# Optimization experiments

Measured on AMD Instinct MI355X. Metric: run time of the kernel, lower is better.

## Reference

```python
import jax, jax.numpy as jnp
import numpy as np

N_NODES = 50000
N_EDGES = 1600000
IN_CH = 128
OUT_CH = 32
HEADS = 4
NEG_SLOPE = 0.2

def setup_inputs() -> dict:
    key = jax.random.key(0)
    ks = jax.random.split(key, 6)
    x = jax.random.normal(ks[0], (N_NODES, IN_CH), dtype=jnp.float32)
    edge_index = jax.random.randint(ks[1], (2, N_EDGES), 0, N_NODES, dtype=jnp.int64)
    # GATConv parameters (glorot-ish scale)
    W = jax.random.normal(ks[2], (IN_CH, HEADS * OUT_CH), dtype=jnp.float32) * (1.0 / np.sqrt(IN_CH))
    att_src = jax.random.normal(ks[3], (HEADS, OUT_CH), dtype=jnp.float32) * (1.0 / np.sqrt(OUT_CH))
    att_dst = jax.random.normal(ks[4], (HEADS, OUT_CH), dtype=jnp.float32) * (1.0 / np.sqrt(OUT_CH))
    bias = jnp.zeros((HEADS * OUT_CH,), dtype=jnp.float32)
    return {"x": x, "edge_index": edge_index, "W": W, "att_src": att_src, "att_dst": att_dst, "bias": bias}

def reference(x, edge_index, W, att_src, att_dst, bias):
    N = x.shape[0]
    H, C = att_src.shape
    # PyG default: add self loops
    loop = jnp.arange(N, dtype=edge_index.dtype)
    src = jnp.concatenate([edge_index[0], loop])  # [E+N]
    dst = jnp.concatenate([edge_index[1], loop])  # [E+N]
    # linear projection -> [N, H, C]
    h = (x @ W).reshape(N, H, C)
    # per-node attention contributions [N, H]
    a_src = jnp.einsum('nhc,hc->nh', h, att_src)
    a_dst = jnp.einsum('nhc,hc->nh', h, att_dst)
    # edge-wise logits with LeakyReLU [E', H]
    alpha = jax.nn.leaky_relu(a_src[src] + a_dst[dst], negative_slope=NEG_SLOPE)
    # segment softmax over incoming edges of each dst node
    amax = jax.ops.segment_max(alpha, dst, num_segments=N)
    alpha = jnp.exp(alpha - amax[dst])
    denom = jax.ops.segment_sum(alpha, dst, num_segments=N)
    alpha = alpha / (denom[dst] + 1e-16)
    # weighted scatter-aggregate of source features [N, H, C]
    msg = h[src] * alpha[..., None]
    out = jax.ops.segment_sum(msg, dst, num_segments=N)
    out = out.reshape(N, H * C) + bias  # concat heads + bias
    return out, alpha
```

## Files before the change

### kernel.cpp

```cpp
#include <hip/hip_runtime.h>
#include <math.h>

#define N_NODES 50000
#define N_EDGES 1600000
#define E_TOT   1650000
#define GROWS   32
#define GEMM_BLOCKS ((N_NODES + GROWS - 1) / GROWS)
#define STRIDE  72
#define NBKT    391
#define PPART   450
#define EPB     3556
#define CAP     32
#define NALPHA  ((E_TOT + 255) / 256)

__device__ __forceinline__ unsigned short f2bf(float f) {
    unsigned int b = __float_as_uint(f);
    return (unsigned short)((b + 0x7FFFu + ((b >> 16) & 1u)) >> 16);
}
__device__ __forceinline__ float bf_lo(unsigned int u) {
    return __uint_as_float(u << 16);
}
__device__ __forceinline__ float bf_hi(unsigned int u) {
    return __uint_as_float(u & 0xFFFF0000u);
}

__global__ __launch_bounds__(256) void k_gemm_part(
    const float* __restrict__ x, const float* __restrict__ W,
    const float* __restrict__ att_src, const float* __restrict__ att_dst,
    unsigned short* __restrict__ hbuf16, float* __restrict__ asrc,
    float* __restrict__ adst,
    const int* __restrict__ esrc, const int* __restrict__ edst,
    unsigned int* __restrict__ cells, int* __restrict__ cellCnt)
{
    __shared__ float  xs[GROWS * 128];
    __shared__ float4 Wl[64 * 32];
    __shared__ int    cur[NBKT];
    const int tid = threadIdx.x;

    if (blockIdx.x >= PPART) {
        const int n0 = (blockIdx.x - PPART) * GROWS;

        {
            const float4* xg = (const float4*)x;
            float4* xs4 = (float4*)xs;
            #pragma unroll
            for (int i = 0; i < 4; i++) {
                int idx = tid + 256 * i;
                int row = n0 + (idx >> 5);
                int col = idx & 31;
                row = min(row, N_NODES - 1);
                xs4[idx] = xg[(size_t)row * 32 + col];
            }
        }

        const int ct = tid & 31;
        const int rt = tid >> 5;
        const int rb = rt * 4;

        float acc[4][4];
        #pragma unroll
        for (int r = 0; r < 4; r++)
            #pragma unroll
            for (int q = 0; q < 4; q++) acc[r][q] = 0.f;

        const float4* W4  = (const float4*)W;
        const float4* xs4 = (const float4*)xs;
        #pragma unroll
        for (int kc = 0; kc < 2; kc++) {
            const float4* Wg = W4 + kc * 2048;
            __syncthreads();
            #pragma unroll
            for (int i = 0; i < 8; i++)
                Wl[tid + 256 * i] = Wg[tid + 256 * i];
            __syncthreads();

            const int kq = kc * 16;
            #pragma unroll 2
            for (int k4 = 0; k4 < 16; k4++) {
                float4 w0 = Wl[(k4 * 4 + 0) * 32 + ct];
                float4 w1 = Wl[(k4 * 4 + 1) * 32 + ct];
                float4 w2 = Wl[(k4 * 4 + 2) * 32 + ct];
                float4 w3 = Wl[(k4 * 4 + 3) * 32 + ct];
                #pragma unroll
                for (int r = 0; r < 4; r++) {
                    float4 xv = xs4[(rb + r) * 32 + kq + k4];
                    acc[r][0] = fmaf(xv.x, w0.x, acc[r][0]);
                    acc[r][1] = fmaf(xv.x, w0.y, acc[r][1]);
                    acc[r][2] = fmaf(xv.x, w0.z, acc[r][2]);
                    acc[r][3] = fmaf(xv.x, w0.w, acc[r][3]);
                    acc[r][0] = fmaf(xv.y, w1.x, acc[r][0]);
                    acc[r][1] = fmaf(xv.y, w1.y, acc[r][1]);
                    acc[r][2] = fmaf(xv.y, w1.z, acc[r][2]);
                    acc[r][3] = fmaf(xv.y, w1.w, acc[r][3]);
                    acc[r][0] = fmaf(xv.z, w2.x, acc[r][0]);
                    acc[r][1] = fmaf(xv.z, w2.y, acc[r][1]);
                    acc[r][2] = fmaf(xv.z, w2.z, acc[r][2]);
                    acc[r][3] = fmaf(xv.z, w2.w, acc[r][3]);
                    acc[r][0] = fmaf(xv.w, w3.x, acc[r][0]);
                    acc[r][1] = fmaf(xv.w, w3.y, acc[r][1]);
                    acc[r][2] = fmaf(xv.w, w3.z, acc[r][2]);
                    acc[r][3] = fmaf(xv.w, w3.w, acc[r][3]);
                }
            }
        }

        ushort4* h4 = (ushort4*)hbuf16;
        #pragma unroll
        for (int r = 0; r < 4; r++) {
            int row = n0 + rb + r;
            if (row < N_NODES) {
                ushort4 p;
                p.x = f2bf(acc[r][0]); p.y = f2bf(acc[r][1]);
                p.z = f2bf(acc[r][2]); p.w = f2bf(acc[r][3]);
                h4[(size_t)row * 32 + ct] = p;
            }
        }

        const int head = ct >> 3;
        const int c0   = (ct & 7) * 4;
        const float* As = att_src + head * 32 + c0;
        const float* Ad = att_dst + head * 32 + c0;
        float sv[4], dv[4];
        #pragma unroll
        for (int r = 0; r < 4; r++) {
            sv[r] = acc[r][0]*As[0] + acc[r][1]*As[1] + acc[r][2]*As[2] + acc[r][3]*As[3];
            dv[r] = acc[r][0]*Ad[0] + acc[r][1]*Ad[1] + acc[r][2]*Ad[2] + acc[r][3]*Ad[3];
        }
        #pragma unroll
        for (int off = 4; off >= 1; off >>= 1) {
            #pragma unroll
            for (int r = 0; r < 4; r++) {
                sv[r] += __shfl_down(sv[r], off, 8);
                dv[r] += __shfl_down(dv[r], off, 8);
            }
        }
        if ((ct & 7) == 0) {
            #pragma unroll
            for (int r = 0; r < 4; r++) {
                int row = n0 + rb + r;
                if (row < N_NODES) {
                    asrc[row * 4 + head] = sv[r];
                    adst[row * 4 + head] = dv[r];
                }
            }
        }
    } else {
        const int p = blockIdx.x;
        for (int i = tid; i < NBKT; i += 256) cur[i] = 0;
        __syncthreads();

        const int base = p * EPB;
        const int end  = min(base + EPB, N_EDGES);
        unsigned int* myCells = cells + (size_t)p * NBKT * CAP;
        for (int e = base + tid; e < end; e += 256) {
            int d = edst[e];
            int s = esrc[e];
            int bkt = d >> 7;
            int pos = atomicAdd(&cur[bkt], 1);
            if (pos < CAP)
                myCells[bkt * CAP + pos] = ((unsigned int)(d & 127) << 16) | (unsigned int)s;
        }
        __syncthreads();
        for (int i = tid; i < NBKT; i += 256)
            cellCnt[p * NBKT + i] = min(cur[i], CAP);
    }
}

__global__ __launch_bounds__(512) void k_build(
    const unsigned int* __restrict__ cells, const int* __restrict__ cellCnt,
    const float4* __restrict__ asrc, const float4* __restrict__ adst,
    int* __restrict__ csr, int* __restrict__ cnt, float4* __restrict__ rden)
{
    __shared__ int cur[128];
    __shared__ int scnt[PPART];
    __shared__ __align__(16) int rows[128 * STRIDE];

    const int tid = threadIdx.x;
    const int b   = blockIdx.x;
    const int d0  = b * 128;
    const int ndst = min(128, N_NODES - d0);
    for (int i = tid; i < 128; i += 512) cur[i] = 0;
    for (int i = tid; i < PPART; i += 512) scnt[i] = cellCnt[i * NBKT + b];
    __syncthreads();

    for (int slot = tid; slot < PPART * CAP; slot += 512) {
        int p = slot >> 5;
        int j = slot & 31;
        if (j < scnt[p]) {
            unsigned int v = cells[((size_t)p * NBKT + b) * CAP + j];
            int dlo = (int)(v >> 16);
            int s   = (int)(v & 0xFFFFu);
            int r = atomicAdd(&cur[dlo], 1);
            if (r < STRIDE) rows[dlo * STRIDE + r] = s;
        }
    }
    __syncthreads();

    int4* dst4 = (int4*)(csr + (size_t)d0 * STRIDE);
    const int4* src4 = (const int4*)rows;
    const int n4 = ndst * (STRIDE / 4);
    for (int k = tid; k < n4; k += 512) dst4[k] = src4[k];
    for (int t = tid; t < ndst; t += 512) cnt[d0 + t] = min(cur[t], STRIDE);

    const int g = tid >> 5, l = tid & 31;
    for (int dd = g; dd < ndst; dd += 16) {
        const int dn = d0 + dd;
        const float4 b4 = adst[dn];
        const int c = min(cur[dd], STRIDE);
        float4 dp = make_float4(0.f, 0.f, 0.f, 0.f);
        for (int i = l; i <= c; i += 32) {
            int s = (i < c) ? rows[dd * STRIDE + i] : dn;
            float4 a4 = asrc[s];
            float l0=a4.x+b4.x, l1=a4.y+b4.y, l2=a4.z+b4.z, l3=a4.w+b4.w;
            l0=fmaxf(l0,0.2f*l0); l1=fmaxf(l1,0.2f*l1);
            l2=fmaxf(l2,0.2f*l2); l3=fmaxf(l3,0.2f*l3);
            dp.x += __expf(l0); dp.y += __expf(l1);
            dp.z += __expf(l2); dp.w += __expf(l3);
        }
        #pragma unroll
        for (int o = 16; o >= 1; o >>= 1) {
            dp.x += __shfl_down(dp.x, o, 32);
            dp.y += __shfl_down(dp.y, o, 32);
            dp.z += __shfl_down(dp.z, o, 32);
            dp.w += __shfl_down(dp.w, o, 32);
        }
        if (l == 0) {
            float4 r;
            r.x = 1.0f / (dp.x + 1e-16f);
            r.y = 1.0f / (dp.y + 1e-16f);
            r.z = 1.0f / (dp.z + 1e-16f);
            r.w = 1.0f / (dp.w + 1e-16f);
            rden[dn] = r;
        }
    }
}

__global__ __launch_bounds__(64) void k_gather_alpha(
    const int* __restrict__ csr, const int* __restrict__ esrc,
    const int* __restrict__ edst, const float4* __restrict__ asrc,
    const float4* __restrict__ adst, const uint4* __restrict__ hbuf4,
    const int* __restrict__ cnt, const float* __restrict__ bias,
    const float4* __restrict__ rden, float4* __restrict__ alpha,
    float4* __restrict__ out4)
{
    __shared__ float4 lds_ex[STRIDE + 1];
    __shared__ int    lds_s[STRIDE + 1];

    const int tid = threadIdx.x;

    if (blockIdx.x < NALPHA) {
        const int base = blockIdx.x * 256;
        #pragma unroll
        for (int i = 0; i < 4; i++) {
            int e = base + i * 64 + tid;
            if (e < E_TOT) {
                int s, d;
                if (e < N_EDGES) { s = esrc[e]; d = edst[e]; }
                else             { s = e - N_EDGES; d = s; }
                float4 a4 = asrc[s];
                float4 b4 = adst[d];
                float4 r4 = rden[d];
                float l0=a4.x+b4.x, l1=a4.y+b4.y, l2=a4.z+b4.z, l3=a4.w+b4.w;
                l0=fmaxf(l0,0.2f*l0); l1=fmaxf(l1,0.2f*l1);
                l2=fmaxf(l2,0.2f*l2); l3=fmaxf(l3,0.2f*l3);
                float4 w;
                w.x = __expf(l0) * r4.x;
                w.y = __expf(l1) * r4.y;
                w.z = __expf(l2) * r4.z;
                w.w = __expf(l3) * r4.w;
                alpha[e] = w;
            }
        }
        return;
    }

    const int d    = blockIdx.x - NALPHA;
    const int c    = cnt[d];
    const int ctot = c + 1;
    const float4 b4 = adst[d];
    const float4 r4 = rden[d];
    const int* row = csr + (size_t)d * STRIDE;

    for (int i = tid; i < ctot; i += 64) {
        int s = (i < c) ? row[i] : d;
        float4 a4 = asrc[s];
        float l0=a4.x+b4.x, l1=a4.y+b4.y, l2=a4.z+b4.z, l3=a4.w+b4.w;
        l0=fmaxf(l0,0.2f*l0); l1=fmaxf(l1,0.2f*l1);
        l2=fmaxf(l2,0.2f*l2); l3=fmaxf(l3,0.2f*l3);
        float4 w;
        w.x = __expf(l0) * r4.x;
        w.y = __expf(l1) * r4.y;
        w.z = __expf(l2) * r4.z;
        w.w = __expf(l3) * r4.w;
        lds_ex[i] = w;
        lds_s[i]  = s;
    }
    __syncthreads();

    const int lane16 = tid & 15;
    const int q      = tid >> 4;
    const int head   = lane16 >> 2;

    float a0=0.f,a1=0.f,a2=0.f,a3=0.f,a4=0.f,a5=0.f,a6=0.f,a7=0.f;
    for (int j = q; j < ctot; j += 4) {
        float w = ((const float*)&lds_ex[j])[head];
        int   s = lds_s[j];
        uint4 hv = hbuf4[(size_t)s * 16 + lane16];
        a0 = fmaf(w, bf_lo(hv.x), a0);
        a1 = fmaf(w, bf_hi(hv.x), a1);
        a2 = fmaf(w, bf_lo(hv.y), a2);
        a3 = fmaf(w, bf_hi(hv.y), a3);
        a4 = fmaf(w, bf_lo(hv.z), a4);
        a5 = fmaf(w, bf_hi(hv.z), a5);
        a6 = fmaf(w, bf_lo(hv.w), a6);
        a7 = fmaf(w, bf_hi(hv.w), a7);
    }
    a0 += __shfl_down(a0, 32, 64); a1 += __shfl_down(a1, 32, 64);
    a2 += __shfl_down(a2, 32, 64); a3 += __shfl_down(a3, 32, 64);
    a4 += __shfl_down(a4, 32, 64); a5 += __shfl_down(a5, 32, 64);
    a6 += __shfl_down(a6, 32, 64); a7 += __shfl_down(a7, 32, 64);
    a0 += __shfl_down(a0, 16, 64); a1 += __shfl_down(a1, 16, 64);
    a2 += __shfl_down(a2, 16, 64); a3 += __shfl_down(a3, 16, 64);
    a4 += __shfl_down(a4, 16, 64); a5 += __shfl_down(a5, 16, 64);
    a6 += __shfl_down(a6, 16, 64); a7 += __shfl_down(a7, 16, 64);
    if (tid < 16) {
        float4 bb0 = ((const float4*)bias)[lane16 * 2];
        float4 bb1 = ((const float4*)bias)[lane16 * 2 + 1];
        float4 o0, o1;
        o0.x = a0 + bb0.x; o0.y = a1 + bb0.y; o0.z = a2 + bb0.z; o0.w = a3 + bb0.w;
        o1.x = a4 + bb1.x; o1.y = a5 + bb1.y; o1.z = a6 + bb1.z; o1.w = a7 + bb1.w;
        out4[(size_t)d * 32 + lane16 * 2]     = o0;
        out4[(size_t)d * 32 + lane16 * 2 + 1] = o1;
    }
}

extern "C" void kernel_launch(void* const* d_in, const int* in_sizes, int n_in,
                              void* d_out, int out_size, void* d_ws, size_t ws_size,
                              hipStream_t stream)
{
    const float* x       = (const float*)d_in[0];
    const int*   ei      = (const int*)d_in[1];
    const float* W       = (const float*)d_in[2];
    const float* att_src = (const float*)d_in[3];
    const float* att_dst = (const float*)d_in[4];
    const float* bias    = (const float*)d_in[5];

    const int* esrc = ei;
    const int* edst = ei + N_EDGES;

    float* out   = (float*)d_out;
    float* alpha = out + (size_t)N_NODES * 128;

    unsigned short* hbuf16 = (unsigned short*)d_ws;
    float* asrc  = (float*)(hbuf16 + (size_t)N_NODES * 128);
    float* adst  = asrc + N_NODES * 4;
    float* rden  = adst + N_NODES * 4;
    int*   cnt   = (int*)(rden + N_NODES * 4);
    int*   csr   = cnt + N_NODES;
    unsigned int* cells = (unsigned int*)(csr + (size_t)N_NODES * STRIDE);
    int*   cellCnt = (int*)(cells + (size_t)PPART * NBKT * CAP);

    k_gemm_part<<<PPART + GEMM_BLOCKS, 256, 0, stream>>>(
        x, W, att_src, att_dst, hbuf16, asrc, adst,
        esrc, edst, cells, cellCnt);

    k_build<<<NBKT, 512, 0, stream>>>(cells, cellCnt,
                                      (const float4*)asrc, (const float4*)adst,
                                      csr, cnt, (float4*)rden);

    k_gather_alpha<<<NALPHA + N_NODES, 64, 0, stream>>>(
        csr, esrc, edst, (const float4*)asrc, (const float4*)adst,
        (const uint4*)hbuf16, cnt, bias, (const float4*)rden,
        (float4*)alpha, (float4*)out);
}
```

Measured before the change: 223.4 us.

## Enlarge GEMM row tile, union shared memory, pack adst with rden, reorder blocks

Doubles the rows per GEMM block so each thread accumulates 8 rows, reusing each loaded W tile across more rows. Shared memory is unioned between the GEMM and partition branches. k_build now writes adst and the reciprocal denominator interleaved into one packed array, so the gather kernel fetches both with adjacent loads. The gather kernel also schedules the per-node aggregation blocks ahead of the edge alpha blocks. Larger tiles raise register pressure and LDS use, which could lower occupancy.

```diff
diff --git a/kernel.cpp b/kernel.cpp
--- a/kernel.cpp
+++ b/kernel.cpp
@@ -4,7 +4,7 @@
 #define N_NODES 50000
 #define N_EDGES 1600000
 #define E_TOT   1650000
-#define GROWS   32
+#define GROWS   64
 #define GEMM_BLOCKS ((N_NODES + GROWS - 1) / GROWS)
 #define STRIDE  72
 #define NBKT    391
@@ -32,19 +32,18 @@
     const int* __restrict__ esrc, const int* __restrict__ edst,
     unsigned int* __restrict__ cells, int* __restrict__ cellCnt)
 {
-    __shared__ float  xs[GROWS * 128];
-    __shared__ float4 Wl[64 * 32];
-    __shared__ int    cur[NBKT];
+    __shared__ __align__(16) char smem[GROWS * 128 * 4 + 64 * 32 * 16];
     const int tid = threadIdx.x;
 
     if (blockIdx.x >= PPART) {
+        float4* xs4 = (float4*)smem;
+        float4* Wl  = (float4*)(smem + GROWS * 128 * 4);
         const int n0 = (blockIdx.x - PPART) * GROWS;
 
         {
             const float4* xg = (const float4*)x;
-            float4* xs4 = (float4*)xs;
-            #pragma unroll
-            for (int i = 0; i < 4; i++) {
+            #pragma unroll
+            for (int i = 0; i < 8; i++) {
                 int idx = tid + 256 * i;
                 int row = n0 + (idx >> 5);
                 int col = idx & 31;
@@ -55,16 +54,15 @@
 
         const int ct = tid & 31;
         const int rt = tid >> 5;
-        const int rb = rt * 4;
-
-        float acc[4][4];
-        #pragma unroll
-        for (int r = 0; r < 4; r++)
+        const int rb = rt * 8;
+
+        float acc[8][4];
+        #pragma unroll
+        for (int r = 0; r < 8; r++)
             #pragma unroll
             for (int q = 0; q < 4; q++) acc[r][q] = 0.f;
 
-        const float4* W4  = (const float4*)W;
-        const float4* xs4 = (const float4*)xs;
+        const float4* W4 = (const float4*)W;
         #pragma unroll
         for (int kc = 0; kc < 2; kc++) {
             const float4* Wg = W4 + kc * 2048;
@@ -75,14 +73,13 @@
             __syncthreads();
 
             const int kq = kc * 16;
-            #pragma unroll 2
             for (int k4 = 0; k4 < 16; k4++) {
                 float4 w0 = Wl[(k4 * 4 + 0) * 32 + ct];
                 float4 w1 = Wl[(k4 * 4 + 1) * 32 + ct];
                 float4 w2 = Wl[(k4 * 4 + 2) * 32 + ct];
                 float4 w3 = Wl[(k4 * 4 + 3) * 32 + ct];
                 #pragma unroll
-                for (int r = 0; r < 4; r++) {
+                for (int r = 0; r < 8; r++) {
                     float4 xv = xs4[(rb + r) * 32 + kq + k4];
                     acc[r][0] = fmaf(xv.x, w0.x, acc[r][0]);
                     acc[r][1] = fmaf(xv.x, w0.y, acc[r][1]);
@@ -106,7 +103,7 @@
 
         ushort4* h4 = (ushort4*)hbuf16;
         #pragma unroll
-        for (int r = 0; r < 4; r++) {
+        for (int r = 0; r < 8; r++) {
             int row = n0 + rb + r;
             if (row < N_NODES) {
                 ushort4 p;
@@ -120,23 +117,23 @@
         const int c0   = (ct & 7) * 4;
         const float* As = att_src + head * 32 + c0;
         const float* Ad = att_dst + head * 32 + c0;
-        float sv[4], dv[4];
-        #pragma unroll
-        for (int r = 0; r < 4; r++) {
+        float sv[8], dv[8];
+        #pragma unroll
+        for (int r = 0; r < 8; r++) {
             sv[r] = acc[r][0]*As[0] + acc[r][1]*As[1] + acc[r][2]*As[2] + acc[r][3]*As[3];
             dv[r] = acc[r][0]*Ad[0] + acc[r][1]*Ad[1] + acc[r][2]*Ad[2] + acc[r][3]*Ad[3];
         }
         #pragma unroll
         for (int off = 4; off >= 1; off >>= 1) {
             #pragma unroll
-            for (int r = 0; r < 4; r++) {
+            for (int r = 0; r < 8; r++) {
                 sv[r] += __shfl_down(sv[r], off, 8);
                 dv[r] += __shfl_down(dv[r], off, 8);
             }
         }
         if ((ct & 7) == 0) {
             #pragma unroll
-            for (int r = 0; r < 4; r++) {
+            for (int r = 0; r < 8; r++) {
                 int row = n0 + rb + r;
                 if (row < N_NODES) {
                     asrc[row * 4 + head] = sv[r];
@@ -145,6 +142,7 @@
             }
         }
     } else {
+        int* cur = (int*)smem;
         const int p = blockIdx.x;
         for (int i = tid; i < NBKT; i += 256) cur[i] = 0;
         __syncthreads();
@@ -169,7 +167,7 @@
 __global__ __launch_bounds__(512) void k_build(
     const unsigned int* __restrict__ cells, const int* __restrict__ cellCnt,
     const float4* __restrict__ asrc, const float4* __restrict__ adst,
-    int* __restrict__ csr, int* __restrict__ cnt, float4* __restrict__ rden)
+    int* __restrict__ csr, int* __restrict__ cnt, float4* __restrict__ dpack)
 {
     __shared__ int cur[128];
     __shared__ int scnt[PPART];
@@ -230,7 +228,8 @@
             r.y = 1.0f / (dp.y + 1e-16f);
             r.z = 1.0f / (dp.z + 1e-16f);
             r.w = 1.0f / (dp.w + 1e-16f);
-            rden[dn] = r;
+            dpack[2 * dn]     = b4;
+            dpack[2 * dn + 1] = r;
         }
     }
 }
@@ -238,18 +237,17 @@
 __global__ __launch_bounds__(64) void k_gather_alpha(
     const int* __restrict__ csr, const int* __restrict__ esrc,
     const int* __restrict__ edst, const float4* __restrict__ asrc,
-    const float4* __restrict__ adst, const uint4* __restrict__ hbuf4,
-    const int* __restrict__ cnt, const float* __restrict__ bias,
-    const float4* __restrict__ rden, float4* __restrict__ alpha,
-    float4* __restrict__ out4)
+    const uint4* __restrict__ hbuf4, const int* __restrict__ cnt,
+    const float* __restrict__ bias, const float4* __restrict__ dpack,
+    float4* __restrict__ alpha, float4* __restrict__ out4)
 {
     __shared__ float4 lds_ex[STRIDE + 1];
     __shared__ int    lds_s[STRIDE + 1];
 
     const int tid = threadIdx.x;
 
-    if (blockIdx.x < NALPHA) {
-        const int base = blockIdx.x * 256;
+    if (blockIdx.x >= N_NODES) {
+        const int base = (blockIdx.x - N_NODES) * 256;
         #pragma unroll
         for (int i = 0; i < 4; i++) {
             int e = base + i * 64 + tid;
@@ -258,8 +256,8 @@
                 if (e < N_EDGES) { s = esrc[e]; d = edst[e]; }
                 else             { s = e - N_EDGES; d = s; }
                 float4 a4 = asrc[s];
-                float4 b4 = adst[d];
-                float4 r4 = rden[d];
+                float4 b4 = dpack[2 * d];
+                float4 r4 = dpack[2 * d + 1];
                 float l0=a4.x+b4.x, l1=a4.y+b4.y, l2=a4.z+b4.z, l3=a4.w+b4.w;
                 l0=fmaxf(l0,0.2f*l0); l1=fmaxf(l1,0.2f*l1);
                 l2=fmaxf(l2,0.2f*l2); l3=fmaxf(l3,0.2f*l3);
@@ -274,11 +272,11 @@
         return;
     }
 
-    const int d    = blockIdx.x - NALPHA;
+    const int d    = blockIdx.x;
     const int c    = cnt[d];
     const int ctot = c + 1;
-    const float4 b4 = adst[d];
-    const float4 r4 = rden[d];
+    const float4 b4 = dpack[2 * d];
+    const float4 r4 = dpack[2 * d + 1];
     const int* row = csr + (size_t)d * STRIDE;
 
     for (int i = tid; i < ctot; i += 64) {
@@ -354,8 +352,8 @@
     unsigned short* hbuf16 = (unsigned short*)d_ws;
     float* asrc  = (float*)(hbuf16 + (size_t)N_NODES * 128);
     float* adst  = asrc + N_NODES * 4;
-    float* rden  = adst + N_NODES * 4;
-    int*   cnt   = (int*)(rden + N_NODES * 4);
+    float* dpack = adst + N_NODES * 4;
+    int*   cnt   = (int*)(dpack + N_NODES * 8);
     int*   csr   = cnt + N_NODES;
     unsigned int* cells = (unsigned int*)(csr + (size_t)N_NODES * STRIDE);
     int*   cellCnt = (int*)(cells + (size_t)PPART * NBKT * CAP);
@@ -366,10 +364,10 @@
 
     k_build<<<NBKT, 512, 0, stream>>>(cells, cellCnt,
                                       (const float4*)asrc, (const float4*)adst,
-                                      csr, cnt, (float4*)rden);
-
-    k_gather_alpha<<<NALPHA + N_NODES, 64, 0, stream>>>(
-        csr, esrc, edst, (const float4*)asrc, (const float4*)adst,
-        (const uint4*)hbuf16, cnt, bias, (const float4*)rden,
+                                      csr, cnt, (float4*)dpack);
+
+    k_gather_alpha<<<N_NODES + NALPHA, 64, 0, stream>>>(
+        csr, esrc, edst, (const float4*)asrc,
+        (const uint4*)hbuf16, cnt, bias, (const float4*)dpack,
         (float4*)alpha, (float4*)out);
 }
```

New measurement: 226.6 us. Within noise of the previous version (+1.4%).
